# Kernel optimization log

Measured on AMD Instinct MI355X. Metric: run time of the kernel, lower is better.

## Reference

```python
import jax, jax.numpy as jnp
import numpy as np

D_MODEL = 1024
N_HEADS = 16
D_HEAD = D_MODEL // N_HEADS
B, T = 2, 2048


def setup_inputs() -> dict:
    key = jax.random.key(0)
    ks = jax.random.split(key, 8)
    s = 1.0 / np.sqrt(D_MODEL)
    return {
        "x": jax.random.normal(ks[0], (B, T, D_MODEL), dtype=jnp.float32),
        "ln_g": jnp.ones((D_MODEL,), jnp.float32),
        "ln_b": jnp.zeros((D_MODEL,), jnp.float32),
        "w_qkv": jax.random.normal(ks[1], (D_MODEL, 3 * D_MODEL), jnp.float32) * s,
        "b_qkv": jnp.zeros((3 * D_MODEL,), jnp.float32),
        "w_gate": jax.random.normal(ks[2], (D_MODEL, D_MODEL), jnp.float32) * s,
        "b_gate": jnp.zeros((D_MODEL,), jnp.float32),
        "w_proj": jax.random.normal(ks[3], (D_MODEL, D_MODEL), jnp.float32) * s,
        "b_proj": jnp.zeros((D_MODEL,), jnp.float32),
    }


def reference(x, ln_g, ln_b, w_qkv, b_qkv, w_gate, b_gate, w_proj, b_proj):
    Bb, Tt, Dd = x.shape
    H, dh = N_HEADS, D_HEAD

    # LayerNorm (eps=1e-5, torch default)
    mu = jnp.mean(x, axis=-1, keepdims=True)
    var = jnp.mean((x - mu) ** 2, axis=-1, keepdims=True)
    x_norm = (x - mu) / jnp.sqrt(var + 1e-5) * ln_g + ln_b

    qkv = x_norm @ w_qkv + b_qkv
    q, k, v = jnp.split(qkv, 3, axis=-1)

    # concept gate on the RAW input x (not x_norm), normalized by its mean
    gate_sig = jax.nn.sigmoid(x @ w_gate + b_gate)
    gate_norm = gate_sig / (jnp.mean(gate_sig, axis=-1, keepdims=True) + 1e-5)
    q = q * gate_norm
    k = k * gate_norm

    # [B,T,D] -> [B,H,T,dh]
    def to_heads(t):
        return t.reshape(Bb, Tt, H, dh).transpose(0, 2, 1, 3)

    q, k, v = to_heads(q), to_heads(k), to_heads(v)

    q = jax.nn.elu(q) + 1.0
    k = jax.nn.elu(k) + 1.0

    # materialized outer-product cumsum (faithful to source formulation)
    kv = jnp.einsum("bhtd,bhtm->bhtdm", k, v)          # [B,H,T,dh,dh]
    kv_cumsum = jnp.cumsum(kv, axis=2)
    out_num = jnp.einsum("bhtd,bhtdm->bhtm", q, kv_cumsum)
    k_cumsum = jnp.cumsum(k, axis=2)
    out_den = jnp.einsum("bhtd,bhtd->bht", q, k_cumsum)[..., None] + 1e-5
    out = out_num / out_den                              # [B,H,T,dh]

    out = out.transpose(0, 2, 1, 3).reshape(Bb, Tt, Dd)
    return out @ w_proj + b_proj
```

## Files before the change

### kernel.cpp

```cpp
#include <hip/hip_runtime.h>
#include <math.h>

constexpr int D      = 1024;
constexpr int H      = 16;
constexpr int DH     = 64;
constexpr int Bb     = 2;
constexpr int T      = 2048;
constexpr int BT     = Bb * T;
constexpr int CHUNK  = 64;
constexpr int NC     = T / CHUNK;
constexpr int LS     = 70;

typedef __attribute__((ext_vector_type(8))) short bf16x8;
typedef __attribute__((ext_vector_type(4))) float f32x4;

#define GLOAD_LDS16(gp, lp) \
    __builtin_amdgcn_global_load_lds((const __attribute__((address_space(1))) void*)(gp), \
                                     (__attribute__((address_space(3))) void*)(lp), 16, 0, 0)

__device__ __forceinline__ short to_bf16(float f) {
    unsigned u = __float_as_uint(f);
    unsigned r = (u + 0x7fffu + ((u >> 16) & 1u)) >> 16;
    return (short)r;
}
__device__ __forceinline__ float bf2f(short s) {
    return __uint_as_float(((unsigned)(unsigned short)s) << 16);
}

__device__ __forceinline__ float elu1(float x) {
    return x > 0.0f ? x + 1.0f : __expf(x);
}


__global__ __launch_bounds__(256) void pre_kernel(const float* __restrict__ x,
                                                  const float* __restrict__ g,
                                                  const float* __restrict__ b,
                                                  const float* __restrict__ wq,
                                                  const float* __restrict__ wg,
                                                  const float* __restrict__ wp,
                                                  short* __restrict__ ynb,
                                                  short* __restrict__ xbb,
                                                  short* __restrict__ wTcomb,
                                                  short* __restrict__ wTp,
                                                  float* __restrict__ gmean) {
    __shared__ short tile[32][33];
    int bid = blockIdx.x;
    if (bid < 1024) {
        int row  = bid * 4 + (threadIdx.x >> 6);
        int lane = threadIdx.x & 63;
        const float* xr = x + (size_t)row * D;
        float4 xv[4];
        float s = 0.0f;
        #pragma unroll
        for (int i = 0; i < 4; ++i) {
            xv[i] = *(const float4*)(xr + i * 256 + lane * 4);
            s += xv[i].x + xv[i].y + xv[i].z + xv[i].w;
        }
        #pragma unroll
        for (int off = 32; off > 0; off >>= 1) s += __shfl_xor(s, off, 64);
        float mu = s * (1.0f / D);
        float vs = 0.0f;
        #pragma unroll
        for (int i = 0; i < 4; ++i) {
            float d0 = xv[i].x - mu, d1 = xv[i].y - mu;
            float d2 = xv[i].z - mu, d3 = xv[i].w - mu;
            vs += d0 * d0 + d1 * d1 + d2 * d2 + d3 * d3;
        }
        #pragma unroll
        for (int off = 32; off > 0; off >>= 1) vs += __shfl_xor(vs, off, 64);
        float rstd = rsqrtf(vs * (1.0f / D) + 1e-5f);
        if (lane == 0) gmean[row] = 0.0f;
        #pragma unroll
        for (int i = 0; i < 4; ++i) {
            int cc = i * 256 + lane * 4;
            float4 gv = *(const float4*)(g + cc);
            float4 bv = *(const float4*)(b + cc);
            short4 o, xo;
            o.x = to_bf16((xv[i].x - mu) * rstd * gv.x + bv.x);
            o.y = to_bf16((xv[i].y - mu) * rstd * gv.y + bv.y);
            o.z = to_bf16((xv[i].z - mu) * rstd * gv.z + bv.z);
            o.w = to_bf16((xv[i].w - mu) * rstd * gv.w + bv.w);
            xo.x = to_bf16(xv[i].x); xo.y = to_bf16(xv[i].y);
            xo.z = to_bf16(xv[i].z); xo.w = to_bf16(xv[i].w);
            *(short4*)(ynb + (size_t)row * D + cc) = o;
            *(short4*)(xbb + (size_t)row * D + cc) = xo;
        }
    } else {
        int t2 = bid - 1024;
        const float* W; short* Wt; int N; int t;
        if (t2 < 3072)      { W = wq; Wt = wTcomb;                       N = 3072; t = t2; }
        else if (t2 < 4096) { W = wg; Wt = wTcomb + (size_t)3072 * 1024; N = 1024; t = t2 - 3072; }
        else                { W = wp; Wt = wTp;                          N = 1024; t = t2 - 4096; }
        int ntiles = N >> 5;
        int nb = (t % ntiles) * 32, kb = (t / ntiles) * 32;
        int tx = threadIdx.x & 31, ty = threadIdx.x >> 5;
        #pragma unroll
        for (int i = 0; i < 4; ++i) {
            int k = kb + ty + i * 8;
            tile[ty + i * 8][tx] = to_bf16(W[(size_t)k * N + nb + tx]);
        }
        __syncthreads();
        #pragma unroll
        for (int i = 0; i < 4; ++i) {
            int n = nb + ty + i * 8;
            Wt[(size_t)n * 1024 + kb + tx] = tile[tx][ty + i * 8];
        }
    }
}

#define SWZ(os) ((os) ^ ((((os) >> 6) & 3) << 3))
#define BARX() __builtin_amdgcn_s_barrier()
#define LGKM0() asm volatile("s_waitcnt lgkmcnt(0)" ::: "memory")
#define VMW(n) asm volatile("s_waitcnt vmcnt(" #n ")" ::: "memory")
#define MEMFENCE() asm volatile("" ::: "memory")

#define STG(Mp, rb, t, kc, isB) do {                                                       \
    short* _b = ldsbuf + ((((t) & 1)) << 15) + (((((isB) << 1) | (kc))) << 13) + wid * 1024; \
    const short* _g = (Mp) + (size_t)((rb) + wid * 32 + s_r) * 1024 + (t) * 64 + (kc) * 32 + s_c; \
    GLOAD_LDS16(_g, _b);                                                                   \
    GLOAD_LDS16(_g + (size_t)16 * 1024, _b + 512);                                         \
} while (0)

#define FRAGA(t, kc, mi) (*(const bf16x8*)(ldsbuf + (((t) & 1) << 15) + ((kc) << 13) + \
    SWZ((wm * 128 + (mi) * 16 + fr) * 32 + fk)))
#define FRAGB(t, kc, ni) (*(const bf16x8*)(ldsbuf + (((t) & 1) << 15) + ((2 + (kc)) << 13) + \
    SWZ((wn * 64 + (ni) * 16 + fr) * 32 + fk)))

#define GROUP(t, S1, S2, S3, S4, W2, W4) do {                                              \
    bf16x8 af[8], bq[4];                                                                   \
    _Pragma("unroll") for (int mi = 0; mi < 8; ++mi) af[mi] = FRAGA(t, 0, mi);             \
    bq[0] = FRAGB(t, 0, 0); bq[1] = FRAGB(t, 0, 1);                                        \
    if (S1) STG(Wt, col0, (t) + 1, 1, 1);                                                  \
    BARX(); LGKM0();                                                                       \
    __builtin_amdgcn_s_setprio(1);                                                         \
    _Pragma("unroll") for (int mi = 0; mi < 8; ++mi) {                                     \
        acc[mi][0] = __builtin_amdgcn_mfma_f32_16x16x32_bf16(af[mi], bq[0], acc[mi][0], 0, 0, 0); \
        acc[mi][1] = __builtin_amdgcn_mfma_f32_16x16x32_bf16(af[mi], bq[1], acc[mi][1], 0, 0, 0); \
    }                                                                                      \
    __builtin_amdgcn_s_setprio(0);                                                         \
    BARX();                                                                                \
    bq[2] = FRAGB(t, 0, 2); bq[3] = FRAGB(t, 0, 3);                                        \
    if (S2) STG(Ap, row0, (t) + 2, 0, 0);                                                  \
    BARX(); LGKM0();                                                                       \
    __builtin_amdgcn_s_setprio(1);                                                         \
    _Pragma("unroll") for (int mi = 0; mi < 8; ++mi) {                                     \
        acc[mi][2] = __builtin_amdgcn_mfma_f32_16x16x32_bf16(af[mi], bq[2], acc[mi][2], 0, 0, 0); \
        acc[mi][3] = __builtin_amdgcn_mfma_f32_16x16x32_bf16(af[mi], bq[3], acc[mi][3], 0, 0, 0); \
    }                                                                                      \
    __builtin_amdgcn_s_setprio(0);                                                         \
    W2; BARX();                                                                            \
    _Pragma("unroll") for (int mi = 0; mi < 8; ++mi) af[mi] = FRAGA(t, 1, mi);             \
    bq[0] = FRAGB(t, 1, 0); bq[1] = FRAGB(t, 1, 1);                                        \
    if (S3) STG(Wt, col0, (t) + 2, 0, 1);                                                  \
    BARX(); LGKM0();                                                                       \
    __builtin_amdgcn_s_setprio(1);                                                         \
    _Pragma("unroll") for (int mi = 0; mi < 8; ++mi) {                                     \
        acc[mi][0] = __builtin_amdgcn_mfma_f32_16x16x32_bf16(af[mi], bq[0], acc[mi][0], 0, 0, 0); \
        acc[mi][1] = __builtin_amdgcn_mfma_f32_16x16x32_bf16(af[mi], bq[1], acc[mi][1], 0, 0, 0); \
    }                                                                                      \
    __builtin_amdgcn_s_setprio(0);                                                         \
    BARX();                                                                                \
    bq[2] = FRAGB(t, 1, 2); bq[3] = FRAGB(t, 1, 3);                                        \
    if (S4) STG(Ap, row0, (t) + 2, 1, 0);                                                  \
    BARX(); LGKM0();                                                                       \
    __builtin_amdgcn_s_setprio(1);                                                         \
    _Pragma("unroll") for (int mi = 0; mi < 8; ++mi) {                                     \
        acc[mi][2] = __builtin_amdgcn_mfma_f32_16x16x32_bf16(af[mi], bq[2], acc[mi][2], 0, 0, 0); \
        acc[mi][3] = __builtin_amdgcn_mfma_f32_16x16x32_bf16(af[mi], bq[3], acc[mi][3], 0, 0, 0); \
    }                                                                                      \
    __builtin_amdgcn_s_setprio(0);                                                         \
    W4; BARX();                                                                            \
} while (0)

__global__ __launch_bounds__(512, 2) void gemm_fused_qkvgate(const short* __restrict__ xnb,
                                                             const short* __restrict__ xb,
                                                             const short* __restrict__ Wt,
                                                             const float* __restrict__ b_qkv,
                                                             const float* __restrict__ b_gate,
                                                             short* __restrict__ qkvb,
                                                             short* __restrict__ sigb,
                                                             float* __restrict__ gmean) {
    __shared__ short ldsbuf[2 * 32768];

    const int bid   = blockIdx.x;
    const int xcd   = bid & 7;
    const int local = bid >> 3;
    const int cx = xcd & 3, ry = xcd >> 2;
    const int bxx = cx * 4 + (local & 3);
    const int byy = ry * 8 + (local >> 2);
    const int row0 = byy * 256;
    const int col0 = bxx * 256;
    const bool isg = (col0 >= 3 * D);
    const short* Ap = isg ? xb : xnb;

    const int tid  = threadIdx.x;
    const int wid  = tid >> 6;
    const int lane = tid & 63;
    const int wm = wid >> 2;
    const int wn = wid & 3;
    const int fr = lane & 15;
    const int fk = (lane >> 4) * 8;

    const int s_r = lane >> 2;
    const int s_c = 8 * ((lane & 3) ^ ((lane >> 3) & 3));

    f32x4 acc[8][4] = {};

    STG(Ap, row0, 0, 0, 0); MEMFENCE();
    STG(Wt, col0, 0, 0, 1); MEMFENCE();
    STG(Ap, row0, 0, 1, 0); MEMFENCE();
    STG(Wt, col0, 0, 1, 1); MEMFENCE();
    STG(Ap, row0, 1, 0, 0); MEMFENCE();
    STG(Wt, col0, 1, 0, 1); MEMFENCE();
    STG(Ap, row0, 1, 1, 0);
    VMW(10);
    BARX();

    for (int t = 0; t < 14; ++t) GROUP(t, 1, 1, 1, 1, VMW(10), VMW(10));
    GROUP(14, 1, 0, 0, 0, VMW(8), VMW(4));
    GROUP(15, 0, 0, 0, 0, VMW(0), (void)0);

    const int ccol  = lane & 15;
    const int crow4 = (lane >> 4) * 4;
    if (!isg) {
        #pragma unroll
        for (int mi = 0; mi < 8; ++mi) {
            #pragma unroll
            for (int ni = 0; ni < 4; ++ni) {
                int col = col0 + wn * 64 + ni * 16 + ccol;
                float bv = b_qkv[col];
                #pragma unroll
                for (int r = 0; r < 4; ++r) {
                    int row = row0 + wm * 128 + mi * 16 + crow4 + r;
                    qkvb[(size_t)row * (3 * D) + col] = to_bf16(acc[mi][ni][r] + bv);
                }
            }
        }
    } else {
        #pragma unroll
        for (int mi = 0; mi < 8; ++mi) {
            #pragma unroll
            for (int r = 0; r < 4; ++r) {
                int lrow = row0 + wm * 128 + mi * 16 + crow4 + r;
                float psum = 0.0f;
                #pragma unroll
                for (int ni = 0; ni < 4; ++ni) {
                    int col = col0 + wn * 64 + ni * 16 + ccol - 3 * D;
                    float v = acc[mi][ni][r] + b_gate[col];
                    float sv = 1.0f / (1.0f + __expf(-v));
                    sigb[(size_t)lrow * D + col] = to_bf16(sv);
                    psum += sv;
                }
                psum += __shfl_xor(psum, 1, 64);
                psum += __shfl_xor(psum, 2, 64);
                psum += __shfl_xor(psum, 4, 64);
                psum += __shfl_xor(psum, 8, 64);
                if (ccol == 0) atomicAdd(&gmean[lrow], psum);
            }
        }
    }
}

__global__ __launch_bounds__(256) void chunk_state_mfma(const short* __restrict__ qkvb,
                                                        const short* __restrict__ sigb,
                                                        const float* __restrict__ gmean,
                                                        float* __restrict__ Sc,
                                                        float* __restrict__ zc) {
    __shared__ short Kt[DH * LS];
    __shared__ short Vt[DH * LS];
    int idx = blockIdx.x;
    int c = idx & (NC - 1), h = (idx >> 5) & (H - 1), b = idx >> 9;
    size_t bt0 = (size_t)b * T + c * CHUNK;
    const short* kbase = qkvb + bt0 * (3 * D) + D + h * DH;
    const short* vbase = kbase + D;
    const short* sbase = sigb + bt0 * D + h * DH;
    int tid = threadIdx.x;

    #pragma unroll
    for (int l = 0; l < 2; ++l) {
        int i  = tid + l * 256;
        int t  = i >> 3;
        int d8 = (i & 7) * 8;
        float invm = 1.0f / (gmean[bt0 + t] * (1.0f / D) + 1e-5f);
        bf16x8 kv = *(const bf16x8*)(kbase + (size_t)t * (3 * D) + d8);
        bf16x8 vv = *(const bf16x8*)(vbase + (size_t)t * (3 * D) + d8);
        bf16x8 sg = *(const bf16x8*)(sbase + (size_t)t * D + d8);
        #pragma unroll
        for (int j = 0; j < 8; ++j) {
            float gn = bf2f(sg[j]) * invm;
            Kt[(d8 + j) * LS + t] = to_bf16(elu1(bf2f(kv[j]) * gn));
            Vt[(d8 + j) * LS + t] = vv[j];
        }
    }
    __syncthreads();

    const int wv = tid >> 6, lane = tid & 63;
    const int fr = lane & 15, quad = lane >> 4;
    const int fk = quad * 8, crow4 = quad * 4, ccol = lane & 15;
    const int mbase = wv * 16;

    bf16x8 af0 = *(const bf16x8*)&Vt[(mbase + fr) * LS + fk];
    bf16x8 af1 = *(const bf16x8*)&Vt[(mbase + fr) * LS + 32 + fk];

    f32x4 acc[4] = {};
    #pragma unroll
    for (int n = 0; n < 4; ++n) {
        bf16x8 bk0 = *(const bf16x8*)&Kt[(n * 16 + fr) * LS + fk];
        bf16x8 bk1 = *(const bf16x8*)&Kt[(n * 16 + fr) * LS + 32 + fk];
        acc[n] = __builtin_amdgcn_mfma_f32_16x16x32_bf16(af0, bk0, acc[n], 0, 0, 0);
        acc[n] = __builtin_amdgcn_mfma_f32_16x16x32_bf16(af1, bk1, acc[n], 0, 0, 0);
    }

    float* Sd = Sc + (size_t)idx * (DH * DH);
    #pragma unroll
    for (int n = 0; n < 4; ++n)
        #pragma unroll
        for (int r = 0; r < 4; ++r)
            Sd[(mbase + crow4 + r) * DH + n * 16 + ccol] = acc[n][r];

    {
        int d = tid >> 2, p = tid & 3;
        bf16x8 k0 = *(const bf16x8*)&Kt[d * LS + p * 16];
        bf16x8 k1 = *(const bf16x8*)&Kt[d * LS + p * 16 + 8];
        float zs = 0.0f;
        #pragma unroll
        for (int j = 0; j < 8; ++j) zs += bf2f(k0[j]) + bf2f(k1[j]);
        zs += __shfl_xor(zs, 1, 64);
        zs += __shfl_xor(zs, 2, 64);
        if (p == 0) zc[(size_t)idx * DH + d] = zs;
    }
}

__global__ __launch_bounds__(256) void chunk_attn_mfma(const short* __restrict__ qkvb,
                                                       const short* __restrict__ sigb,
                                                       const float* __restrict__ gmean,
                                                       const float* __restrict__ Sc,
                                                       const float* __restrict__ zc,
                                                       short* __restrict__ attnb) {
    __shared__ short Qs[CHUNK * LS];
    __shared__ short Ks[CHUNK * LS];
    __shared__ short Vt[DH * LS];
    __shared__ short Ss[DH * LS];
    __shared__ float zpL[DH];
    __shared__ float den[CHUNK];
    short* As = Ks;

    int idx = blockIdx.x;
    int c = idx & (NC - 1), h = (idx >> 5) & (H - 1), b = idx >> 9;
    size_t bt0 = (size_t)b * T + c * CHUNK;
    const short* qbase = qkvb + bt0 * (3 * D) + h * DH;
    const short* kbase = qbase + D;
    const short* vbase = qbase + 2 * D;
    const short* sbase = sigb + bt0 * D + h * DH;
    int tid = threadIdx.x;

    #pragma unroll
    for (int l = 0; l < 2; ++l) {
        int i  = tid + l * 256;
        int t  = i >> 3;
        int d8 = (i & 7) * 8;
        float invm = 1.0f / (gmean[bt0 + t] * (1.0f / D) + 1e-5f);
        bf16x8 qv = *(const bf16x8*)(qbase + (size_t)t * (3 * D) + d8);
        bf16x8 kv = *(const bf16x8*)(kbase + (size_t)t * (3 * D) + d8);
        bf16x8 vv = *(const bf16x8*)(vbase + (size_t)t * (3 * D) + d8);
        bf16x8 sg = *(const bf16x8*)(sbase + (size_t)t * D + d8);
        bf16x8 qg, kg;
        #pragma unroll
        for (int j = 0; j < 8; ++j) {
            float gn = bf2f(sg[j]) * invm;
            qg[j] = to_bf16(elu1(bf2f(qv[j]) * gn));
            kg[j] = to_bf16(elu1(bf2f(kv[j]) * gn));
            Vt[(d8 + j) * LS + t] = vv[j];
        }
        *(bf16x8*)&Qs[t * LS + d8] = qg;
        *(bf16x8*)&Ks[t * LS + d8] = kg;
    }

    {
        const float* Sb = Sc + (size_t)(idx & ~(NC - 1)) * (DH * DH) + tid * 16;
        f32x4 a0 = {}, a1 = {}, a2 = {}, a3 = {};
        for (int cc = 0; cc < c; ++cc) {
            const float* p = Sb + (size_t)cc * (DH * DH);
            a0 += *(const f32x4*)(p);
            a1 += *(const f32x4*)(p + 4);
            a2 += *(const f32x4*)(p + 8);
            a3 += *(const f32x4*)(p + 12);
        }
        int m = tid >> 2, d0 = (tid & 3) * 16;
        bf16x8 s0, s1;
        #pragma unroll
        for (int j = 0; j < 4; ++j) { s0[j] = to_bf16(a0[j]); s0[4 + j] = to_bf16(a1[j]); }
        #pragma unroll
        for (int j = 0; j < 4; ++j) { s1[j] = to_bf16(a2[j]); s1[4 + j] = to_bf16(a3[j]); }
        *(bf16x8*)&Ss[m * LS + d0]     = s0;
        *(bf16x8*)&Ss[m * LS + d0 + 8] = s1;
    }
    if (tid < DH) {
        const float* zb = zc + (size_t)(idx & ~(NC - 1)) * DH + tid;
        float zp = 0.0f;
        for (int cc = 0; cc < c; ++cc) zp += zb[(size_t)cc * DH];
        zpL[tid] = zp;
    }
    __syncthreads();

    const int wv = tid >> 6, lane = tid & 63;
    const int fr = lane & 15, quad = lane >> 4;
    const int fk = quad * 8, crow4 = quad * 4, ccol = lane & 15;
    const int tbase = wv * 16;

    bf16x8 aq0 = *(const bf16x8*)&Qs[(tbase + fr) * LS + fk];
    bf16x8 aq1 = *(const bf16x8*)&Qs[(tbase + fr) * LS + 32 + fk];

    f32x4 accs[4] = {};
    #pragma unroll
    for (int n = 0; n < 4; ++n) {
        bf16x8 bk0 = *(const bf16x8*)&Ks[(n * 16 + fr) * LS + fk];
        bf16x8 bk1 = *(const bf16x8*)&Ks[(n * 16 + fr) * LS + 32 + fk];
        accs[n] = __builtin_amdgcn_mfma_f32_16x16x32_bf16(aq0, bk0, accs[n], 0, 0, 0);
        accs[n] = __builtin_amdgcn_mfma_f32_16x16x32_bf16(aq1, bk1, accs[n], 0, 0, 0);
    }
    __syncthreads();

    float part[4] = {0.f, 0.f, 0.f, 0.f};
    #pragma unroll
    for (int n = 0; n < 4; ++n) {
        #pragma unroll
        for (int r = 0; r < 4; ++r) {
            int tt = tbase + crow4 + r;
            int ss = n * 16 + ccol;
            float v = (ss <= tt) ? accs[n][r] : 0.0f;
            part[r] += v;
            As[tt * LS + ss] = to_bf16(v);
        }
    }
    #pragma unroll
    for (int r = 0; r < 4; ++r) {
        part[r] += __shfl_xor(part[r], 1, 64);
        part[r] += __shfl_xor(part[r], 2, 64);
        part[r] += __shfl_xor(part[r], 4, 64);
        part[r] += __shfl_xor(part[r], 8, 64);
    }
    if (fr == 0) {
        #pragma unroll
        for (int r = 0; r < 4; ++r) den[tbase + crow4 + r] = part[r];
    }
    __syncthreads();

    {
        int t = tid >> 2, p = tid & 3;
        bf16x8 q0 = *(const bf16x8*)&Qs[t * LS + p * 16];
        bf16x8 q1 = *(const bf16x8*)&Qs[t * LS + p * 16 + 8];
        float qz = 0.0f;
        #pragma unroll
        for (int j = 0; j < 8; ++j)
            qz += bf2f(q0[j]) * zpL[p * 16 + j] + bf2f(q1[j]) * zpL[p * 16 + 8 + j];
        qz += __shfl_xor(qz, 1, 64);
        qz += __shfl_xor(qz, 2, 64);
        if (p == 0) den[t] += qz + 1e-5f;
    }

    f32x4 acco[4] = {};
    #pragma unroll
    for (int m4 = 0; m4 < 4; ++m4) {
        bf16x8 bs0 = *(const bf16x8*)&Ss[(m4 * 16 + fr) * LS + fk];
        bf16x8 bs1 = *(const bf16x8*)&Ss[(m4 * 16 + fr) * LS + 32 + fk];
        acco[m4] = __builtin_amdgcn_mfma_f32_16x16x32_bf16(aq0, bs0, acco[m4], 0, 0, 0);
        acco[m4] = __builtin_amdgcn_mfma_f32_16x16x32_bf16(aq1, bs1, acco[m4], 0, 0, 0);
    }
    bf16x8 aa0 = *(const bf16x8*)&As[(tbase + fr) * LS + fk];
    bf16x8 aa1 = *(const bf16x8*)&As[(tbase + fr) * LS + 32 + fk];
    #pragma unroll
    for (int m4 = 0; m4 < 4; ++m4) {
        bf16x8 bv0 = *(const bf16x8*)&Vt[(m4 * 16 + fr) * LS + fk];
        bf16x8 bv1 = *(const bf16x8*)&Vt[(m4 * 16 + fr) * LS + 32 + fk];
        acco[m4] = __builtin_amdgcn_mfma_f32_16x16x32_bf16(aa0, bv0, acco[m4], 0, 0, 0);
        acco[m4] = __builtin_amdgcn_mfma_f32_16x16x32_bf16(aa1, bv1, acco[m4], 0, 0, 0);
    }
    __syncthreads();

    short* obase = attnb + bt0 * D + h * DH;
    #pragma unroll
    for (int r = 0; r < 4; ++r) {
        int tt = tbase + crow4 + r;
        float rv = 1.0f / den[tt];
        #pragma unroll
        for (int m4 = 0; m4 < 4; ++m4)
            obase[(size_t)tt * D + m4 * 16 + ccol] = to_bf16(acco[m4][r] * rv);
    }
}

#define SWZ64(os) ((os) ^ ((((os) >> 6) & 7) << 3))

__global__ __launch_bounds__(256) void gemm_proj64(const short* __restrict__ A,
                                                   const short* __restrict__ Bt,
                                                   const float* __restrict__ bias,
                                                   float* __restrict__ C) {
    constexpr int BK = 64, K = 1024;
    constexpr int N = 1024;
    __shared__ short Als[64 * BK];
    __shared__ short Bls[128 * BK];

    const int bid   = blockIdx.x;
    const int xcd   = bid & 7;
    const int local = bid >> 3;
    const int cx = xcd & 3, ry = xcd >> 2;
    const int lx = local & 1, ly = local >> 1;
    const int bxx = cx * 2 + lx;
    const int byy = ry * 32 + ly;

    const int tid  = threadIdx.x;
    const int wave = tid >> 6;
    const int lane = tid & 63;
    const int row0 = byy * 64;
    const int col0 = bxx * 128;
    const int wn = wave * 32;

    f32x4 acc[4][2] = {};
    const int fr = lane & 15;
    const int fk = (lane >> 4) * 8;

    for (int k0 = 0; k0 < K; k0 += BK) {
        __syncthreads();
        #pragma unroll
        for (int u = 0; u < 2; ++u) {
            int slot = tid + u * 256;
            int r = slot >> 3, c8 = (slot & 7) ^ (r & 7);
            GLOAD_LDS16(A + (size_t)(row0 + r) * K + k0 + c8 * 8, &Als[slot * 8]);
        }
        #pragma unroll
        for (int u = 0; u < 4; ++u) {
            int slot = tid + u * 256;
            int r = slot >> 3, c8 = (slot & 7) ^ (r & 7);
            GLOAD_LDS16(Bt + (size_t)(col0 + r) * K + k0 + c8 * 8, &Bls[slot * 8]);
        }
        __syncthreads();

        #pragma unroll
        for (int ck = 0; ck < 2; ++ck) {
            bf16x8 af[4], bfr[2];
            #pragma unroll
            for (int i = 0; i < 4; ++i)
                af[i] = *(const bf16x8*)&Als[SWZ64((i * 16 + fr) * BK + ck * 32 + fk)];
            #pragma unroll
            for (int j = 0; j < 2; ++j)
                bfr[j] = *(const bf16x8*)&Bls[SWZ64((wn + j * 16 + fr) * BK + ck * 32 + fk)];
            #pragma unroll
            for (int mi = 0; mi < 4; ++mi)
                #pragma unroll
                for (int ni = 0; ni < 2; ++ni)
                    acc[mi][ni] = __builtin_amdgcn_mfma_f32_16x16x32_bf16(af[mi], bfr[ni], acc[mi][ni], 0, 0, 0);
        }
    }

    const int ccol  = lane & 15;
    const int crow4 = (lane >> 4) * 4;
    #pragma unroll
    for (int mi = 0; mi < 4; ++mi) {
        #pragma unroll
        for (int ni = 0; ni < 2; ++ni) {
            int col = col0 + wn + ni * 16 + ccol;
            float bv = bias[col];
            #pragma unroll
            for (int r = 0; r < 4; ++r) {
                int row = row0 + mi * 16 + crow4 + r;
                C[(size_t)row * N + col] = acc[mi][ni][r] + bv;
            }
        }
    }
}

extern "C" void kernel_launch(void* const* d_in, const int* in_sizes, int n_in,
                              void* d_out, int out_size, void* d_ws, size_t ws_size,
                              hipStream_t stream) {
    const float* x      = (const float*)d_in[0];
    const float* ln_g   = (const float*)d_in[1];
    const float* ln_b   = (const float*)d_in[2];
    const float* w_qkv  = (const float*)d_in[3];
    const float* b_qkv  = (const float*)d_in[4];
    const float* w_gate = (const float*)d_in[5];
    const float* b_gate = (const float*)d_in[6];
    const float* w_proj = (const float*)d_in[7];
    const float* b_proj = (const float*)d_in[8];
    float* out = (float*)d_out;

    short* xnb   = (short*)d_ws;
    short* xb    = xnb + (size_t)BT * D;
    short* wTc   = xb + (size_t)BT * D;
    short* wTp   = wTc + (size_t)4096 * 1024;
    short* qkvb  = wTp + (size_t)D * D;
    short* sigb  = qkvb + (size_t)BT * 3 * D;
    short* attnb = sigb + (size_t)BT * D;
    float* zc    = (float*)(attnb + (size_t)BT * D);
    float* gmean = zc + (size_t)Bb * H * NC * DH;
    float* Sc    = (float*)xnb;

    pre_kernel<<<1024 + 5120, 256, 0, stream>>>(x, ln_g, ln_b, w_qkv, w_gate, w_proj,
                                                xnb, xb, wTc, wTp, gmean);
    gemm_fused_qkvgate<<<256, 512, 0, stream>>>(
        xnb, xb, wTc, b_qkv, b_gate, qkvb, sigb, gmean);
    chunk_state_mfma<<<Bb * H * NC, 256, 0, stream>>>(qkvb, sigb, gmean, Sc, zc);
    chunk_attn_mfma<<<Bb * H * NC, 256, 0, stream>>>(qkvb, sigb, gmean, Sc, zc, attnb);
    gemm_proj64<<<512, 256, 0, stream>>>(attnb, wTp, b_proj, out);
}
```

Baseline: 204.5 us.

## Precompute chunk-state prefix sums in a separate kernel and widen weight transpose tiles

Adds a chunk_prefix_kernel that computes exclusive prefix sums of the per-chunk KV states and key sums once, storing the states as bf16. chunk_attn_mfma then loads its prefix state directly instead of re-summing up to 31 fp32 chunk states per block, which removes quadratic redundant global reads. The weight transpose in pre_kernel now uses 64x64 tiles with vectorized float4 loads and bf16x8 stores, and the LDS stride changes from 70 to 72. The cost is one extra kernel launch and an extra round trip of the prefix state through memory, which reuses the wTc buffer after the QKV GEMM is done with it.

```diff
diff --git a/kernel.cpp b/kernel.cpp
--- a/kernel.cpp
+++ b/kernel.cpp
@@ -9,7 +9,7 @@
 constexpr int BT     = Bb * T;
 constexpr int CHUNK  = 64;
 constexpr int NC     = T / CHUNK;
-constexpr int LS     = 70;
+constexpr int LS     = 72;
 
 typedef __attribute__((ext_vector_type(8))) short bf16x8;
 typedef __attribute__((ext_vector_type(4))) float f32x4;
@@ -43,11 +43,12 @@
                                                   short* __restrict__ wTcomb,
                                                   short* __restrict__ wTp,
                                                   float* __restrict__ gmean) {
-    __shared__ short tile[32][33];
+    __shared__ short tile2[64 * 72];
     int bid = blockIdx.x;
+    int tid = threadIdx.x;
     if (bid < 1024) {
-        int row  = bid * 4 + (threadIdx.x >> 6);
-        int lane = threadIdx.x & 63;
+        int row  = bid * 4 + (tid >> 6);
+        int lane = tid & 63;
         const float* xr = x + (size_t)row * D;
         float4 xv[4];
         float s = 0.0f;
@@ -88,23 +89,38 @@
     } else {
         int t2 = bid - 1024;
         const float* W; short* Wt; int N; int t;
-        if (t2 < 3072)      { W = wq; Wt = wTcomb;                       N = 3072; t = t2; }
-        else if (t2 < 4096) { W = wg; Wt = wTcomb + (size_t)3072 * 1024; N = 1024; t = t2 - 3072; }
-        else                { W = wp; Wt = wTp;                          N = 1024; t = t2 - 4096; }
-        int ntiles = N >> 5;
-        int nb = (t % ntiles) * 32, kb = (t / ntiles) * 32;
-        int tx = threadIdx.x & 31, ty = threadIdx.x >> 5;
-        #pragma unroll
-        for (int i = 0; i < 4; ++i) {
-            int k = kb + ty + i * 8;
-            tile[ty + i * 8][tx] = to_bf16(W[(size_t)k * N + nb + tx]);
-        }
+        if (t2 < 768)       { W = wq; Wt = wTcomb;                       N = 3072; t = t2; }
+        else if (t2 < 1024) { W = wg; Wt = wTcomb + (size_t)3072 * 1024; N = 1024; t = t2 - 768; }
+        else                { W = wp; Wt = wTp;                          N = 1024; t = t2 - 1024; }
+        int ntn = N >> 6;
+        int nb = (t % ntn) * 64, kb = (t / ntn) * 64;
+
+        int k  = tid >> 2;
+        int n4 = (tid & 3) * 16;
+        const float* src = W + (size_t)(kb + k) * N + nb + n4;
+        float4 f0 = *(const float4*)(src);
+        float4 f1 = *(const float4*)(src + 4);
+        float4 f2 = *(const float4*)(src + 8);
+        float4 f3 = *(const float4*)(src + 12);
+        bf16x8 h0, h1;
+        h0[0] = to_bf16(f0.x); h0[1] = to_bf16(f0.y); h0[2] = to_bf16(f0.z); h0[3] = to_bf16(f0.w);
+        h0[4] = to_bf16(f1.x); h0[5] = to_bf16(f1.y); h0[6] = to_bf16(f1.z); h0[7] = to_bf16(f1.w);
+        h1[0] = to_bf16(f2.x); h1[1] = to_bf16(f2.y); h1[2] = to_bf16(f2.z); h1[3] = to_bf16(f2.w);
+        h1[4] = to_bf16(f3.x); h1[5] = to_bf16(f3.y); h1[6] = to_bf16(f3.z); h1[7] = to_bf16(f3.w);
+        *(bf16x8*)&tile2[k * 72 + n4]     = h0;
+        *(bf16x8*)&tile2[k * 72 + n4 + 8] = h1;
         __syncthreads();
-        #pragma unroll
-        for (int i = 0; i < 4; ++i) {
-            int n = nb + ty + i * 8;
-            Wt[(size_t)n * 1024 + kb + tx] = tile[tx][ty + i * 8];
-        }
+
+        int n   = tid >> 2;
+        int k16 = (tid & 3) * 16;
+        bf16x8 o0, o1;
+        #pragma unroll
+        for (int j = 0; j < 8; ++j) o0[j] = tile2[(k16 + j) * 72 + n];
+        #pragma unroll
+        for (int j = 0; j < 8; ++j) o1[j] = tile2[(k16 + 8 + j) * 72 + n];
+        short* dst = Wt + (size_t)(nb + n) * 1024 + kb + k16;
+        *(bf16x8*)dst       = o0;
+        *(bf16x8*)(dst + 8) = o1;
     }
 }
 
@@ -331,10 +347,41 @@
     }
 }
 
+__global__ __launch_bounds__(256) void chunk_prefix_kernel(const float* __restrict__ S,
+                                                           short* __restrict__ Spb,
+                                                           float* __restrict__ z) {
+    int bh   = blockIdx.x >> 4;
+    int part = blockIdx.x & 15;
+    int e    = part * 256 + threadIdx.x;
+    const float* Sb = S + (size_t)bh * NC * DH * DH;
+    short* Pb = Spb + (size_t)bh * NC * DH * DH;
+    float v[NC];
+    #pragma unroll
+    for (int c = 0; c < NC; ++c) v[c] = Sb[(size_t)c * DH * DH + e];
+    float acc = 0.0f;
+    #pragma unroll
+    for (int c = 0; c < NC; ++c) {
+        Pb[(size_t)c * DH * DH + e] = to_bf16(acc);
+        acc += v[c];
+    }
+    if (part == 0 && threadIdx.x < DH) {
+        float* zb = z + (size_t)bh * NC * DH + threadIdx.x;
+        float zv[NC];
+        #pragma unroll
+        for (int c = 0; c < NC; ++c) zv[c] = zb[(size_t)c * DH];
+        float za = 0.0f;
+        #pragma unroll
+        for (int c = 0; c < NC; ++c) {
+            zb[(size_t)c * DH] = za;
+            za += zv[c];
+        }
+    }
+}
+
 __global__ __launch_bounds__(256) void chunk_attn_mfma(const short* __restrict__ qkvb,
                                                        const short* __restrict__ sigb,
                                                        const float* __restrict__ gmean,
-                                                       const float* __restrict__ Sc,
+                                                       const short* __restrict__ Spb,
                                                        const float* __restrict__ zc,
                                                        short* __restrict__ attnb) {
     __shared__ short Qs[CHUNK * LS];
@@ -352,6 +399,7 @@
     const short* kbase = qbase + D;
     const short* vbase = qbase + 2 * D;
     const short* sbase = sigb + bt0 * D + h * DH;
+    const short* spb = Spb + (size_t)idx * (DH * DH);
     int tid = threadIdx.x;
 
     #pragma unroll
@@ -374,33 +422,9 @@
         }
         *(bf16x8*)&Qs[t * LS + d8] = qg;
         *(bf16x8*)&Ks[t * LS + d8] = kg;
-    }
-
-    {
-        const float* Sb = Sc + (size_t)(idx & ~(NC - 1)) * (DH * DH) + tid * 16;
-        f32x4 a0 = {}, a1 = {}, a2 = {}, a3 = {};
-        for (int cc = 0; cc < c; ++cc) {
-            const float* p = Sb + (size_t)cc * (DH * DH);
-            a0 += *(const f32x4*)(p);
-            a1 += *(const f32x4*)(p + 4);
-            a2 += *(const f32x4*)(p + 8);
-            a3 += *(const f32x4*)(p + 12);
-        }
-        int m = tid >> 2, d0 = (tid & 3) * 16;
-        bf16x8 s0, s1;
-        #pragma unroll
-        for (int j = 0; j < 4; ++j) { s0[j] = to_bf16(a0[j]); s0[4 + j] = to_bf16(a1[j]); }
-        #pragma unroll
-        for (int j = 0; j < 4; ++j) { s1[j] = to_bf16(a2[j]); s1[4 + j] = to_bf16(a3[j]); }
-        *(bf16x8*)&Ss[m * LS + d0]     = s0;
-        *(bf16x8*)&Ss[m * LS + d0 + 8] = s1;
-    }
-    if (tid < DH) {
-        const float* zb = zc + (size_t)(idx & ~(NC - 1)) * DH + tid;
-        float zp = 0.0f;
-        for (int cc = 0; cc < c; ++cc) zp += zb[(size_t)cc * DH];
-        zpL[tid] = zp;
-    }
+        *(bf16x8*)&Ss[t * LS + d8] = *(const bf16x8*)(spb + (size_t)i * 8);
+    }
+    if (tid < DH) zpL[tid] = zc[(size_t)idx * DH + tid];
     __syncthreads();
 
     const int wv = tid >> 6, lane = tid & 63;
@@ -593,12 +617,14 @@
     float* zc    = (float*)(attnb + (size_t)BT * D);
     float* gmean = zc + (size_t)Bb * H * NC * DH;
     float* Sc    = (float*)xnb;
-
-    pre_kernel<<<1024 + 5120, 256, 0, stream>>>(x, ln_g, ln_b, w_qkv, w_gate, w_proj,
+    short* Spb   = wTc;
+
+    pre_kernel<<<1024 + 1280, 256, 0, stream>>>(x, ln_g, ln_b, w_qkv, w_gate, w_proj,
                                                 xnb, xb, wTc, wTp, gmean);
     gemm_fused_qkvgate<<<256, 512, 0, stream>>>(
         xnb, xb, wTc, b_qkv, b_gate, qkvb, sigb, gmean);
     chunk_state_mfma<<<Bb * H * NC, 256, 0, stream>>>(qkvb, sigb, gmean, Sc, zc);
-    chunk_attn_mfma<<<Bb * H * NC, 256, 0, stream>>>(qkvb, sigb, gmean, Sc, zc, attnb);
+    chunk_prefix_kernel<<<Bb * H * 16, 256, 0, stream>>>(Sc, Spb, zc);
+    chunk_attn_mfma<<<Bb * H * NC, 256, 0, stream>>>(qkvb, sigb, gmean, Spb, zc, attnb);
     gemm_proj64<<<512, 256, 0, stream>>>(attnb, wTp, b_proj, out);
 }
```

Measured after the change: 186.6 us. -8.7%, faster.
